# Optimization experiments

Measured on AMD Instinct MI355X. Metric: run time of the kernel, lower is better.

The kernel has to match this reference:

```python
import jax, jax.numpy as jnp
import numpy as np

N_FREQ = 256
N_CH = 256
VOCAB = 8192
B, T = 4, 2048


def gauss_proj(x, w, n_freq):
    # FFT over vocab dim, take first n_freq harmonics (skip DC), split real/imag
    X = jnp.fft.rfft(x, axis=-1)[..., 1:n_freq + 1]          # [B,T,n_freq] complex
    X_ri = jnp.concatenate([X.real, X.imag], axis=-1)         # [B,T,2*n_freq]
    return X_ri @ w.T                                         # [B,T,n_channels]


def gauss_synth(h, w, n_freq, V):
    Y_ri = h @ w                                              # [B,T,2*n_freq]
    Y = Y_ri[..., :n_freq] + 1j * Y_ri[..., n_freq:]          # [B,T,n_freq] complex
    full = jnp.zeros(h.shape[:-1] + (V // 2 + 1,), dtype=Y.dtype)
    full = full.at[..., 1:n_freq + 1].set(Y)                  # band-limited spectrum
    return jnp.fft.irfft(full, n=V, axis=-1)                  # [B,T,V]


def setup_inputs() -> dict:
    key = jax.random.key(0)
    ks = jax.random.split(key, 5)
    x = jax.random.normal(ks[0], (B, T, VOCAB), dtype=jnp.float32)
    q_w = jax.random.normal(ks[1], (N_CH, 2 * N_FREQ), dtype=jnp.float32) * 0.02
    k_w = jax.random.normal(ks[2], (N_CH, 2 * N_FREQ), dtype=jnp.float32) * 0.02
    v_w = jax.random.normal(ks[3], (N_CH, 2 * N_FREQ), dtype=jnp.float32) * 0.02
    o_w = jax.random.normal(ks[4], (N_CH, 2 * N_FREQ), dtype=jnp.float32) * 0.02
    decay_logit = jnp.float32(3.0)
    out_scale = jnp.float32(0.1)
    return {"x": x, "q_w": q_w, "k_w": k_w, "v_w": v_w, "o_w": o_w,
            "decay_logit": decay_logit, "out_scale": out_scale}


def reference(x, q_w, k_w, v_w, o_w, decay_logit, out_scale):
    q = gauss_proj(x, q_w, N_FREQ)                            # [B,T,C]
    k = gauss_proj(x, k_w, N_FREQ)
    v = gauss_proj(x, v_w, N_FREQ)
    scores = jnp.einsum('btc,bsc->bts', q, k)                 # [B,T,T]
    decay = jax.nn.sigmoid(decay_logit)
    t = x.shape[1]
    pos = jnp.arange(t)
    # faithful to torch: diff[t,s] = pos[s] - pos[t]
    diff = pos[None, :] - pos[:, None]
    weights = (decay ** jnp.clip(diff.astype(jnp.float32) - 1.0, 0.0)) * (diff > 0)
    scores = scores * weights[None, :, :]
    retrieved = jnp.einsum('bts,bsc->btc', scores, v)         # [B,T,C]
    return gauss_synth(retrieved, o_w, N_FREQ, VOCAB) * out_scale
```

## Files before the change

### kernel.cpp

```cpp
#include <hip/hip_runtime.h>
#include <hip/hip_bf16.h>
#include <cstdint>


typedef unsigned short u16;
typedef short short8 __attribute__((ext_vector_type(8)));
typedef float f32x4 __attribute__((ext_vector_type(4)));
typedef float f4 __attribute__((ext_vector_type(4)));

__device__ __forceinline__ u16 f2bf(float f) {
  union { float f; unsigned u; } v; v.f = f;
  unsigned u = v.u;
  u += 0x7fffu + ((u >> 16) & 1u);
  return (u16)(u >> 16);
}

__device__ __forceinline__ uint2 pack_bf4(f4 v) {
  union { u16 h[4]; uint2 q; } pk;
  pk.h[0] = f2bf(v[0]); pk.h[1] = f2bf(v[1]);
  pk.h[2] = f2bf(v[2]); pk.h[3] = f2bf(v[3]);
  return pk.q;
}

__device__ __forceinline__ void gload_lds16(const void* g, void* l) {
  __builtin_amdgcn_global_load_lds(
      (const __attribute__((address_space(1))) void*)g,
      (__attribute__((address_space(3))) void*)l, 16, 0, 0);
}

__global__ __launch_bounds__(256, 2)
void gemm_g1(const float* __restrict__ A, const u16* __restrict__ B,
             float* __restrict__ P)
{
  constexpr int NN = 512, KK = 8192, KC = 4096;
  constexpr int NT = KC / 32;

  __shared__ u16 As[2][128 * 32] __attribute__((aligned(16)));
  __shared__ u16 Bs[3][128 * 32] __attribute__((aligned(16)));

  const int tid  = threadIdx.x;
  const int wave = tid >> 6, lane = tid & 63;
  const int quad = lane >> 4, l15 = lane & 15;
  const int wm = wave >> 1, wn = wave & 1;

  const int lid = blockIdx.x;
  const int nat = (lid & 7) * 64 + (lid >> 3);
  const int y = nat >> 3, rem = nat & 7;
  const int x = rem & 3, z = rem >> 2;
  const int m0 = y * 128, n0 = x * 128, k00 = z * KC;

  const int loff0 = wave * 2048 + lane * 16;
  const int loff1 = loff0 + 1024;
  const int row0s = loff0 >> 6, kof0 = (loff0 & 63) >> 1;
  const int row1s = loff1 >> 6, kof1 = (loff1 & 63) >> 1;
  const u16* Bp0 = B + (size_t)(n0 + row0s) * KK + k00 + kof0;
  const u16* Bp1 = B + (size_t)(n0 + row1s) * KK + k00 + kof1;

  const int arow8 = tid >> 3;
  const int acol  = (tid & 7) * 4;
  const float* Ap = A + (size_t)(m0 + arow8) * KK + k00 + acol;

  f4 rv0[4], rv1[4];

#define ISSUE_A(RV, T)                                               \
  _Pragma("unroll")                                                  \
  for (int g = 0; g < 4; ++g)                                        \
    RV[g] = *(const f4*)(Ap + (size_t)g * 32 * KK + (size_t)(T) * 32);
#define ISSUE_B(T, SLOT)                                             \
  gload_lds16(Bp0 + (size_t)(T) * 32, (char*)Bs[SLOT] + loff0);      \
  gload_lds16(Bp1 + (size_t)(T) * 32, (char*)Bs[SLOT] + loff1);
#define CONVERT_A(RV, SLOT)                                          \
  _Pragma("unroll")                                                  \
  for (int g = 0; g < 4; ++g)                                        \
    *(uint2*)&As[SLOT][(g * 32 + arow8) * 32 + acol] = pack_bf4(RV[g]);
#define G1_COMPUTE(CUR, BSLOT)                                                   \
  {                                                                              \
    short8 a[4], b[4];                                                           \
    _Pragma("unroll")                                                            \
    for (int i = 0; i < 4; ++i)                                                  \
      a[i] = *(const short8*)&As[CUR][(wm * 64 + i * 16 + l15) * 32 + quad * 8]; \
    _Pragma("unroll")                                                            \
    for (int j = 0; j < 4; ++j)                                                  \
      b[j] = *(const short8*)&Bs[BSLOT][(wn * 64 + j * 16 + l15) * 32 + quad * 8]; \
    _Pragma("unroll")                                                            \
    for (int i = 0; i < 4; ++i)                                                  \
      _Pragma("unroll")                                                          \
      for (int j = 0; j < 4; ++j)                                                \
        acc[i][j] = __builtin_amdgcn_mfma_f32_16x16x32_bf16(a[i], b[j], acc[i][j], 0, 0, 0); \
  }
#define FENCE_BAR()                                                  \
  asm volatile("s_waitcnt vmcnt(6)" ::: "memory");                   \
  asm volatile("s_waitcnt lgkmcnt(0)" ::: "memory");                 \
  __builtin_amdgcn_s_barrier();                                      \
  asm volatile("" ::: "memory");

  ISSUE_A(rv0, 0);
  ISSUE_B(0, 0);
  ISSUE_A(rv1, 1);
  ISSUE_B(1, 1);
  CONVERT_A(rv0, 0);
  FENCE_BAR();

  f32x4 acc[4][4] = {};

#define BODY(T, RV_ISS, RV_CONV)                                     \
  {                                                                  \
    const int t2 = ((T) + 2 < NT) ? (T) + 2 : NT - 1;                \
    ISSUE_A(RV_ISS, t2);                                             \
    ISSUE_B(t2, ((T) + 2) % 3);                                      \
    G1_COMPUTE((T) & 1, (T) % 3);                                    \
    CONVERT_A(RV_CONV, ((T) + 1) & 1);                               \
    FENCE_BAR();                                                     \
  }

  for (int t = 0; t < NT; t += 2) {
    BODY(t, rv0, rv1);
    BODY(t + 1, rv1, rv0);
  }
#undef BODY
#undef FENCE_BAR
#undef G1_COMPUTE
#undef CONVERT_A
#undef ISSUE_B
#undef ISSUE_A

  float* Pz = P + (size_t)z * (8192L * 512);
  #pragma unroll
  for (int i = 0; i < 4; ++i) {
    #pragma unroll
    for (int j = 0; j < 4; ++j) {
      const int rb = m0 + wm * 64 + i * 16 + quad * 4;
      const int cc = n0 + wn * 64 + j * 16 + l15;
      #pragma unroll
      for (int r = 0; r < 4; ++r)
        Pz[(size_t)(rb + r) * NN + cc] = acc[i][j][r];
    }
  }
}

__global__ void reduce_cast(const float* __restrict__ P, u16* __restrict__ Xri) {
  const int i = blockIdx.x * 256 + threadIdx.x;
  const f4 a = ((const f4*)P)[i];
  const f4 b = ((const f4*)(P + 8192L * 512))[i];
  union { u16 h[4]; uint2 q; } pk;
  #pragma unroll
  for (int r = 0; r < 4; ++r) pk.h[r] = f2bf(a[r] + b[r]);
  ((uint2*)Xri)[i] = pk.q;
}

__global__ __launch_bounds__(256, 2)
void gemm_qkvw(const u16* __restrict__ Xri, const u16* __restrict__ Fm,
               const u16* __restrict__ qwb, const u16* __restrict__ kwb,
               const u16* __restrict__ vwb, const u16* __restrict__ owb,
               u16* __restrict__ Qb, u16* __restrict__ Kb,
               u16* __restrict__ Vt, u16* __restrict__ Wot)
{
  constexpr int N = 256, K = 512;
  __shared__ u16 As[128 * 32] __attribute__((aligned(16)));
  __shared__ u16 Bs[128 * 32] __attribute__((aligned(16)));

  const int tid  = threadIdx.x;
  const int wave = tid >> 6, lane = tid & 63;
  const int quad = lane >> 4, l15 = lane & 15;
  const int wm = wave >> 1, wn = wave & 1;
  const int m0 = blockIdx.y * 128, n0 = blockIdx.x * 128;
  const int z  = blockIdx.z;

  const u16* Ab = (z == 3) ? Fm : Xri;
  const u16* Bb = (z == 0) ? qwb : (z == 1) ? kwb : (z == 2) ? vwb : owb;
  const float alpha = (z == 3) ? (2.f / 8192.f) : 1.f;

  f32x4 acc[4][4] = {};

  const int loff0 = wave * 2048 + lane * 16;
  const int loff1 = loff0 + 1024;
  const int row0s = loff0 >> 6, kof0 = (loff0 & 63) >> 1;
  const int row1s = loff1 >> 6, kof1 = (loff1 & 63) >> 1;

  for (int k0 = 0; k0 < K; k0 += 32) {
    __syncthreads();
    gload_lds16(Ab + (size_t)(m0 + row0s) * K + k0 + kof0, (char*)As + loff0);
    gload_lds16(Ab + (size_t)(m0 + row1s) * K + k0 + kof1, (char*)As + loff1);
    gload_lds16(Bb + (size_t)(n0 + row0s) * K + k0 + kof0, (char*)Bs + loff0);
    gload_lds16(Bb + (size_t)(n0 + row1s) * K + k0 + kof1, (char*)Bs + loff1);
    __syncthreads();

    short8 a[4], b[4];
    #pragma unroll
    for (int i = 0; i < 4; ++i)
      a[i] = *(const short8*)&As[(wm * 64 + i * 16 + l15) * 32 + quad * 8];
    #pragma unroll
    for (int j = 0; j < 4; ++j)
      b[j] = *(const short8*)&Bs[(wn * 64 + j * 16 + l15) * 32 + quad * 8];
    #pragma unroll
    for (int i = 0; i < 4; ++i)
      #pragma unroll
      for (int j = 0; j < 4; ++j)
        acc[i][j] = __builtin_amdgcn_mfma_f32_16x16x32_bf16(a[i], b[j], acc[i][j], 0, 0, 0);
  }

  #pragma unroll
  for (int i = 0; i < 4; ++i) {
    #pragma unroll
    for (int j = 0; j < 4; ++j) {
      f32x4 v = acc[i][j];
      const int rb = m0 + wm * 64 + i * 16 + quad * 4;
      const int cc = n0 + wn * 64 + j * 16 + l15;
      if (z == 2) {
        const int bb = rb >> 11, ml = rb & 2047;
        union { u16 h[4]; uint2 q; } pk;
        #pragma unroll
        for (int r = 0; r < 4; ++r) pk.h[r] = f2bf(v[r]);
        *(uint2*)&Vt[((size_t)(bb << 8) + cc) * 2048 + ml] = pk.q;
      } else {
        u16* C = (z == 0) ? Qb : (z == 1) ? Kb : Wot;
        #pragma unroll
        for (int r = 0; r < 4; ++r)
          C[(size_t)(rb + r) * N + cc] = f2bf(v[r] * alpha);
      }
    }
  }
}

template<int EPI, bool AF32>
__global__ __launch_bounds__(256, 2)
void gemm_bt(const void* __restrict__ Av, const u16* __restrict__ B,
             void* __restrict__ Cv, int M, int N, int K,
             long sA, long sB, long sC,
             const float* __restrict__ scal, float alpha)
{
  __shared__ u16 As[128 * 32] __attribute__((aligned(16)));
  __shared__ u16 Bs[128 * 32] __attribute__((aligned(16)));

  const int tid  = threadIdx.x;
  const int wave = tid >> 6, lane = tid & 63;
  const int quad = lane >> 4, l15 = lane & 15;
  const int wm = wave >> 1, wn = wave & 1;
  const int m0 = blockIdx.y * 128, n0 = blockIdx.x * 128;
  const int z  = blockIdx.z;

  const u16*   Ab = (const u16*)Av + (size_t)z * sA;
  const float* Af = (const float*)Av + (size_t)z * sA;
  const u16*   Bb = B + (size_t)z * sB;

  f32x4 acc[4][4] = {};

  const int loff0 = wave * 2048 + lane * 16;
  const int loff1 = loff0 + 1024;
  const int row0s = loff0 >> 6, kof0 = (loff0 & 63) >> 1;
  const int row1s = loff1 >> 6, kof1 = (loff1 & 63) >> 1;

  for (int k0 = 0; k0 < K; k0 += 32) {
    __syncthreads();
    if (AF32) {
      const int row = tid >> 1, half = tid & 1;
      const float* ar = Af + (size_t)(m0 + row) * K + k0 + half * 16;
      f4 p0 = *(const f4*)(ar);
      f4 p1 = *(const f4*)(ar + 4);
      f4 p2 = *(const f4*)(ar + 8);
      f4 p3 = *(const f4*)(ar + 12);
      union { u16 h[16]; uint4 q[2]; } pk;
      #pragma unroll
      for (int e = 0; e < 4; ++e) {
        pk.h[e]      = f2bf(p0[e]);
        pk.h[4 + e]  = f2bf(p1[e]);
        pk.h[8 + e]  = f2bf(p2[e]);
        pk.h[12 + e] = f2bf(p3[e]);
      }
      uint4* dst = (uint4*)&As[row * 32 + half * 16];
      dst[0] = pk.q[0]; dst[1] = pk.q[1];
    } else {
      gload_lds16(Ab + (size_t)(m0 + row0s) * K + k0 + kof0, (char*)As + loff0);
      gload_lds16(Ab + (size_t)(m0 + row1s) * K + k0 + kof1, (char*)As + loff1);
    }
    gload_lds16(Bb + (size_t)(n0 + row0s) * K + k0 + kof0, (char*)Bs + loff0);
    gload_lds16(Bb + (size_t)(n0 + row1s) * K + k0 + kof1, (char*)Bs + loff1);
    __syncthreads();

    short8 a[4], b[4];
    #pragma unroll
    for (int i = 0; i < 4; ++i)
      a[i] = *(const short8*)&As[(wm * 64 + i * 16 + l15) * 32 + quad * 8];
    #pragma unroll
    for (int j = 0; j < 4; ++j)
      b[j] = *(const short8*)&Bs[(wn * 64 + j * 16 + l15) * 32 + quad * 8];
    #pragma unroll
    for (int i = 0; i < 4; ++i)
      #pragma unroll
      for (int j = 0; j < 4; ++j)
        acc[i][j] = __builtin_amdgcn_mfma_f32_16x16x32_bf16(a[i], b[j], acc[i][j], 0, 0, 0);
  }

  float dec_l2 = 0.f, oscale = 1.f;
  if (EPI == 3) {
    float logit = *scal;
    float dec = 1.f / (1.f + expf(-logit));
    dec_l2 = log2f(dec);
  }
  if (EPI == 4) oscale = *scal;

  #pragma unroll
  for (int i = 0; i < 4; ++i) {
    #pragma unroll
    for (int j = 0; j < 4; ++j) {
      f32x4 v = acc[i][j];
      const int rb = m0 + wm * 64 + i * 16 + quad * 4;
      const int cc = n0 + wn * 64 + j * 16 + l15;
      if (EPI == 0) {
        u16* C = (u16*)Cv + (size_t)z * sC;
        #pragma unroll
        for (int r = 0; r < 4; ++r)
          C[(size_t)(rb + r) * N + cc] = f2bf(v[r] * alpha);
      } else if (EPI == 2) {
        u16* C = (u16*)Cv;
        const int bb = rb >> 11, ml = rb & 2047;
        union { u16 h[4]; uint2 q; } pk;
        #pragma unroll
        for (int r = 0; r < 4; ++r) pk.h[r] = f2bf(v[r]);
        *(uint2*)&C[((size_t)(bb << 8) + cc) * 2048 + ml] = pk.q;
      } else if (EPI == 3) {
        u16* C = (u16*)Cv + (size_t)z * sC;
        #pragma unroll
        for (int r = 0; r < 4; ++r) {
          const int d = cc - (rb + r);
          float w = (d > 0) ? exp2f(dec_l2 * (float)(d - 1)) : 0.f;
          C[(size_t)(rb + r) * N + cc] = f2bf(v[r] * w);
        }
      } else if (EPI == 4) {
        float* C = (float*)Cv;
        #pragma unroll
        for (int r = 0; r < 4; ++r)
          C[(size_t)(rb + r) * N + cc] = v[r] * oscale;
      }
    }
  }
}

__global__ void genF_row(u16* Fm) {
  int idx = blockIdx.x * 256 + threadIdx.x;
  int n = idx >> 9, j = idx & 511;
  int k = (j & 255) + 1;
  int ph = (n * k) & 8191;
  float ang = (float)ph * 7.66990393942820795e-4f;
  float s, c; sincosf(ang, &s, &c);
  Fm[idx] = f2bf(j < 256 ? c : -s);
}
__global__ void genF_col(u16* Ft) {
  int idx = blockIdx.x * 256 + threadIdx.x;
  int j = idx >> 13, n = idx & 8191;
  int k = (j & 255) + 1;
  int ph = (n * k) & 8191;
  float ang = (float)ph * 7.66990393942820795e-4f;
  float s, c; sincosf(ang, &s, &c);
  Ft[idx] = f2bf(j < 256 ? c : -s);
}

__global__ void cast_w4(const float* a, const float* b, const float* c, const float* d,
                        u16* oa, u16* ob, u16* oc, u16* od) {
  int i = blockIdx.x * 256 + threadIdx.x;
  oa[i] = f2bf(a[i]); ob[i] = f2bf(b[i]); oc[i] = f2bf(c[i]); od[i] = f2bf(d[i]);
}

extern "C" void kernel_launch(void* const* d_in, const int* in_sizes, int n_in,
                              void* d_out, int out_size, void* d_ws, size_t ws_size,
                              hipStream_t stream)
{
  const float* x  = (const float*)d_in[0];
  const float* qw = (const float*)d_in[1];
  const float* kw = (const float*)d_in[2];
  const float* vw = (const float*)d_in[3];
  const float* ow = (const float*)d_in[4];
  const float* dl = (const float*)d_in[5];
  const float* os = (const float*)d_in[6];
  float* out = (float*)d_out;

  char* W = (char*)d_ws;
  const size_t MB = 1024 * 1024;
  u16* Fm  = (u16*)(W);
  u16* Ft  = (u16*)(W + 8 * MB);
  u16* Xri = (u16*)(W + 16 * MB);
  u16* Qb  = (u16*)(W + 24 * MB);
  u16* Kb  = (u16*)(W + 28 * MB);
  u16* Vt  = (u16*)(W + 32 * MB);
  u16* Wot = (u16*)(W + 36 * MB);
  u16* S   = (u16*)(W + 40 * MB);
  float* P = (float*)(W + 40 * MB);
  u16* R   = (u16*)(W + 72 * MB);
  u16* qwb = (u16*)(W + 76 * MB);
  u16* kwb = qwb + 131072;
  u16* vwb = kwb + 131072;
  u16* owb = vwb + 131072;

  genF_row<<<8192 * 512 / 256, 256, 0, stream>>>(Fm);
  genF_col<<<8192 * 512 / 256, 256, 0, stream>>>(Ft);
  cast_w4<<<131072 / 256, 256, 0, stream>>>(qw, kw, vw, ow, qwb, kwb, vwb, owb);

  gemm_g1<<<512, 256, 0, stream>>>(x, Ft, P);
  reduce_cast<<<4096, 256, 0, stream>>>(P, Xri);

  gemm_qkvw<<<dim3(2, 64, 4), 256, 0, stream>>>(Xri, Fm, qwb, kwb, vwb, owb,
                                                Qb, Kb, Vt, Wot);

  gemm_bt<3, false><<<dim3(16, 16, 4), 256, 0, stream>>>(Qb, Kb, S, 2048, 2048, 256,
                                                         2048L * 256, 2048L * 256, 2048L * 2048, dl, 1.f);
  gemm_bt<0, false><<<dim3(2, 16, 4), 256, 0, stream>>>(S, Vt, R, 2048, 256, 2048,
                                                        2048L * 2048, 256L * 2048, 2048L * 256, nullptr, 1.f);
  gemm_bt<4, false><<<dim3(64, 64, 1), 256, 0, stream>>>(R, Wot, out, 8192, 8192, 256, 0, 0, 0, os, 1.f);
}
```

Baseline: 680.5 us.

## Skip zero triangle in score and retrieval GEMMs; deepen K tile in spectral GEMM

The QK^T score GEMM now skips output tiles below the diagonal, since the causal decay mask makes them zero. The S·V GEMM is replaced by a split-K kernel that starts each row block's K loop at the diagonal, writes fp32 partials and reduces them with a generalized reduce_cast. Separately, the rfft-projection GEMM moves to a 64-wide K tile with XOR-swizzled LDS layout and double buffering of B, reorganizing its load/compute schedule. The changes cut wasted MFMA work and loop overhead, but add an extra reduction pass and reuse the Fm/Ft workspace for partials.

```diff
diff --git a/kernel.cpp b/kernel.cpp
--- a/kernel.cpp
+++ b/kernel.cpp
@@ -33,15 +33,16 @@
              float* __restrict__ P)
 {
   constexpr int NN = 512, KK = 8192, KC = 4096;
-  constexpr int NT = KC / 32;
-
-  __shared__ u16 As[2][128 * 32] __attribute__((aligned(16)));
-  __shared__ u16 Bs[3][128 * 32] __attribute__((aligned(16)));
+  constexpr int NT = KC / 64;
+
+  __shared__ u16 As[2][128 * 64] __attribute__((aligned(16)));
+  __shared__ u16 Bs[2][128 * 64] __attribute__((aligned(16)));
 
   const int tid  = threadIdx.x;
   const int wave = tid >> 6, lane = tid & 63;
   const int quad = lane >> 4, l15 = lane & 15;
   const int wm = wave >> 1, wn = wave & 1;
+  const int swz8 = (l15 & 7) << 3;
 
   const int lid = blockIdx.x;
   const int nat = (lid & 7) * 64 + (lid >> 3);
@@ -49,55 +50,61 @@
   const int x = rem & 3, z = rem >> 2;
   const int m0 = y * 128, n0 = x * 128, k00 = z * KC;
 
-  const int loff0 = wave * 2048 + lane * 16;
-  const int loff1 = loff0 + 1024;
-  const int row0s = loff0 >> 6, kof0 = (loff0 & 63) >> 1;
-  const int row1s = loff1 >> 6, kof1 = (loff1 & 63) >> 1;
-  const u16* Bp0 = B + (size_t)(n0 + row0s) * KK + k00 + kof0;
-  const u16* Bp1 = B + (size_t)(n0 + row1s) * KK + k00 + kof1;
-
-  const int arow8 = tid >> 3;
-  const int acol  = (tid & 7) * 4;
-  const float* Ap = A + (size_t)(m0 + arow8) * KK + k00 + acol;
-
-  f4 rv0[4], rv1[4];
+  const int brow = tid >> 3;
+  const int bswz = ((tid & 7) * 8) ^ (((tid >> 3) & 7) << 3);
+  const u16* Bp = B + (size_t)(n0 + brow) * KK + k00 + bswz;
+  const int bloff = tid * 16;
+
+  const int arow16 = tid >> 4;
+  const int acolf  = (tid & 15) * 4;
+  const float* Ap = A + (size_t)(m0 + arow16) * KK + k00 + acolf;
+  const int awz = ((tid & 15) * 4) ^ (((tid >> 4) & 7) << 3);
+
+  f4 rv0[8], rv1[8];
 
 #define ISSUE_A(RV, T)                                               \
   _Pragma("unroll")                                                  \
-  for (int g = 0; g < 4; ++g)                                        \
-    RV[g] = *(const f4*)(Ap + (size_t)g * 32 * KK + (size_t)(T) * 32);
+  for (int g = 0; g < 8; ++g)                                        \
+    RV[g] = *(const f4*)(Ap + (size_t)g * 16 * KK + (size_t)(T) * 64);
 #define ISSUE_B(T, SLOT)                                             \
-  gload_lds16(Bp0 + (size_t)(T) * 32, (char*)Bs[SLOT] + loff0);      \
-  gload_lds16(Bp1 + (size_t)(T) * 32, (char*)Bs[SLOT] + loff1);
+  _Pragma("unroll")                                                  \
+  for (int h = 0; h < 4; ++h)                                        \
+    gload_lds16(Bp + (size_t)h * 32 * KK + (size_t)(T) * 64,         \
+                (char*)Bs[SLOT] + h * 4096 + bloff);
 #define CONVERT_A(RV, SLOT)                                          \
   _Pragma("unroll")                                                  \
-  for (int g = 0; g < 4; ++g)                                        \
-    *(uint2*)&As[SLOT][(g * 32 + arow8) * 32 + acol] = pack_bf4(RV[g]);
-#define G1_COMPUTE(CUR, BSLOT)                                                   \
-  {                                                                              \
+  for (int g = 0; g < 8; ++g)                                        \
+    *(uint2*)&As[SLOT][(g * 16 + arow16) * 64 + awz] = pack_bf4(RV[g]);
+#define G1_COMPUTE(CUR)                                                          \
+  _Pragma("unroll")                                                              \
+  for (int ks = 0; ks < 2; ++ks) {                                               \
     short8 a[4], b[4];                                                           \
     _Pragma("unroll")                                                            \
     for (int i = 0; i < 4; ++i)                                                  \
-      a[i] = *(const short8*)&As[CUR][(wm * 64 + i * 16 + l15) * 32 + quad * 8]; \
+      a[i] = *(const short8*)&As[CUR][(wm * 64 + i * 16 + l15) * 64 +            \
+                                      ((ks * 32 + quad * 8) ^ swz8)];            \
     _Pragma("unroll")                                                            \
     for (int j = 0; j < 4; ++j)                                                  \
-      b[j] = *(const short8*)&Bs[BSLOT][(wn * 64 + j * 16 + l15) * 32 + quad * 8]; \
+      b[j] = *(const short8*)&Bs[CUR][(wn * 64 + j * 16 + l15) * 64 +            \
+                                      ((ks * 32 + quad * 8) ^ swz8)];            \
     _Pragma("unroll")                                                            \
     for (int i = 0; i < 4; ++i)                                                  \
       _Pragma("unroll")                                                          \
       for (int j = 0; j < 4; ++j)                                                \
         acc[i][j] = __builtin_amdgcn_mfma_f32_16x16x32_bf16(a[i], b[j], acc[i][j], 0, 0, 0); \
   }
+#define SB() __builtin_amdgcn_sched_barrier(0)
 #define FENCE_BAR()                                                  \
-  asm volatile("s_waitcnt vmcnt(6)" ::: "memory");                   \
+  asm volatile("s_waitcnt vmcnt(8)" ::: "memory");                   \
   asm volatile("s_waitcnt lgkmcnt(0)" ::: "memory");                 \
   __builtin_amdgcn_s_barrier();                                      \
   asm volatile("" ::: "memory");
 
   ISSUE_A(rv0, 0);
   ISSUE_B(0, 0);
+  SB();
   ISSUE_A(rv1, 1);
-  ISSUE_B(1, 1);
+  SB();
   CONVERT_A(rv0, 0);
   FENCE_BAR();
 
@@ -106,9 +113,11 @@
 #define BODY(T, RV_ISS, RV_CONV)                                     \
   {                                                                  \
     const int t2 = ((T) + 2 < NT) ? (T) + 2 : NT - 1;                \
+    ISSUE_B((T) + 1 < NT ? (T) + 1 : NT - 1, ((T) + 1) & 1);         \
+    SB();                                                            \
     ISSUE_A(RV_ISS, t2);                                             \
-    ISSUE_B(t2, ((T) + 2) % 3);                                      \
-    G1_COMPUTE((T) & 1, (T) % 3);                                    \
+    SB();                                                            \
+    G1_COMPUTE((T) & 1);                                             \
     CONVERT_A(RV_CONV, ((T) + 1) & 1);                               \
     FENCE_BAR();                                                     \
   }
@@ -119,6 +128,7 @@
   }
 #undef BODY
 #undef FENCE_BAR
+#undef SB
 #undef G1_COMPUTE
 #undef CONVERT_A
 #undef ISSUE_B
@@ -138,14 +148,15 @@
   }
 }
 
-__global__ void reduce_cast(const float* __restrict__ P, u16* __restrict__ Xri) {
+__global__ void reduce_cast(const float* __restrict__ P, u16* __restrict__ O,
+                            int half_f4) {
   const int i = blockIdx.x * 256 + threadIdx.x;
   const f4 a = ((const f4*)P)[i];
-  const f4 b = ((const f4*)(P + 8192L * 512))[i];
+  const f4 b = ((const f4*)P)[i + half_f4];
   union { u16 h[4]; uint2 q; } pk;
   #pragma unroll
   for (int r = 0; r < 4; ++r) pk.h[r] = f2bf(a[r] + b[r]);
-  ((uint2*)Xri)[i] = pk.q;
+  ((uint2*)O)[i] = pk.q;
 }
 
 __global__ __launch_bounds__(256, 2)
@@ -222,13 +233,80 @@
   }
 }
 
-template<int EPI, bool AF32>
+__global__ __launch_bounds__(256, 2)
+void gemm_g5(const u16* __restrict__ S, const u16* __restrict__ Vt,
+             float* __restrict__ P5)
+{
+  constexpr int N = 256, K = 2048;
+  __shared__ u16 As[128 * 32] __attribute__((aligned(16)));
+  __shared__ u16 Bs[128 * 32] __attribute__((aligned(16)));
+
+  const int tid  = threadIdx.x;
+  const int wave = tid >> 6, lane = tid & 63;
+  const int quad = lane >> 4, l15 = lane & 15;
+  const int wm = wave >> 1, wn = wave & 1;
+  const int m0 = blockIdx.y * 128, n0 = blockIdx.x * 128;
+  const int batch = blockIdx.z & 3, half = blockIdx.z >> 2;
+
+  const u16* Ab = S  + (size_t)batch * 2048 * 2048;
+  const u16* Bb = Vt + (size_t)batch * 256 * 2048;
+
+  int kbeg = half * 1024;
+  if (m0 > kbeg) kbeg = m0;
+  const int kend = half * 1024 + 1024;
+
+  f32x4 acc[4][4] = {};
+
+  const int loff0 = wave * 2048 + lane * 16;
+  const int loff1 = loff0 + 1024;
+  const int row0s = loff0 >> 6, kof0 = (loff0 & 63) >> 1;
+  const int row1s = loff1 >> 6, kof1 = (loff1 & 63) >> 1;
+
+  for (int k0 = kbeg; k0 < kend; k0 += 32) {
+    __syncthreads();
+    gload_lds16(Ab + (size_t)(m0 + row0s) * K + k0 + kof0, (char*)As + loff0);
+    gload_lds16(Ab + (size_t)(m0 + row1s) * K + k0 + kof1, (char*)As + loff1);
+    gload_lds16(Bb + (size_t)(n0 + row0s) * K + k0 + kof0, (char*)Bs + loff0);
+    gload_lds16(Bb + (size_t)(n0 + row1s) * K + k0 + kof1, (char*)Bs + loff1);
+    __syncthreads();
+
+    short8 a[4], b[4];
+    #pragma unroll
+    for (int i = 0; i < 4; ++i)
+      a[i] = *(const short8*)&As[(wm * 64 + i * 16 + l15) * 32 + quad * 8];
+    #pragma unroll
+    for (int j = 0; j < 4; ++j)
+      b[j] = *(const short8*)&Bs[(wn * 64 + j * 16 + l15) * 32 + quad * 8];
+    #pragma unroll
+    for (int i = 0; i < 4; ++i)
+      #pragma unroll
+      for (int j = 0; j < 4; ++j)
+        acc[i][j] = __builtin_amdgcn_mfma_f32_16x16x32_bf16(a[i], b[j], acc[i][j], 0, 0, 0);
+  }
+
+  float* Pz = P5 + (size_t)half * (8192L * 256) + (size_t)batch * 2048 * 256;
+  #pragma unroll
+  for (int i = 0; i < 4; ++i) {
+    #pragma unroll
+    for (int j = 0; j < 4; ++j) {
+      const int rb = m0 + wm * 64 + i * 16 + quad * 4;
+      const int cc = n0 + wn * 64 + j * 16 + l15;
+      #pragma unroll
+      for (int r = 0; r < 4; ++r)
+        Pz[(size_t)(rb + r) * N + cc] = acc[i][j][r];
+    }
+  }
+}
+
+template<int EPI, bool AF32, bool TRI>
 __global__ __launch_bounds__(256, 2)
 void gemm_bt(const void* __restrict__ Av, const u16* __restrict__ B,
              void* __restrict__ Cv, int M, int N, int K,
              long sA, long sB, long sC,
              const float* __restrict__ scal, float alpha)
 {
+  if (TRI && blockIdx.x < blockIdx.y) return;
+
   __shared__ u16 As[128 * 32] __attribute__((aligned(16)));
   __shared__ u16 Bs[128 * 32] __attribute__((aligned(16)));
 
@@ -311,13 +389,6 @@
         #pragma unroll
         for (int r = 0; r < 4; ++r)
           C[(size_t)(rb + r) * N + cc] = f2bf(v[r] * alpha);
-      } else if (EPI == 2) {
-        u16* C = (u16*)Cv;
-        const int bb = rb >> 11, ml = rb & 2047;
-        union { u16 h[4]; uint2 q; } pk;
-        #pragma unroll
-        for (int r = 0; r < 4; ++r) pk.h[r] = f2bf(v[r]);
-        *(uint2*)&C[((size_t)(bb << 8) + cc) * 2048 + ml] = pk.q;
       } else if (EPI == 3) {
         u16* C = (u16*)Cv + (size_t)z * sC;
         #pragma unroll
@@ -385,6 +456,7 @@
   u16* Wot = (u16*)(W + 36 * MB);
   u16* S   = (u16*)(W + 40 * MB);
   float* P = (float*)(W + 40 * MB);
+  float* P5 = (float*)(W);
   u16* R   = (u16*)(W + 72 * MB);
   u16* qwb = (u16*)(W + 76 * MB);
   u16* kwb = qwb + 131072;
@@ -396,14 +468,15 @@
   cast_w4<<<131072 / 256, 256, 0, stream>>>(qw, kw, vw, ow, qwb, kwb, vwb, owb);
 
   gemm_g1<<<512, 256, 0, stream>>>(x, Ft, P);
-  reduce_cast<<<4096, 256, 0, stream>>>(P, Xri);
+  reduce_cast<<<4096, 256, 0, stream>>>(P, Xri, 8192 * 512 / 4);
 
   gemm_qkvw<<<dim3(2, 64, 4), 256, 0, stream>>>(Xri, Fm, qwb, kwb, vwb, owb,
                                                 Qb, Kb, Vt, Wot);
 
-  gemm_bt<3, false><<<dim3(16, 16, 4), 256, 0, stream>>>(Qb, Kb, S, 2048, 2048, 256,
-                                                         2048L * 256, 2048L * 256, 2048L * 2048, dl, 1.f);
-  gemm_bt<0, false><<<dim3(2, 16, 4), 256, 0, stream>>>(S, Vt, R, 2048, 256, 2048,
-                                                        2048L * 2048, 256L * 2048, 2048L * 256, nullptr, 1.f);
-  gemm_bt<4, false><<<dim3(64, 64, 1), 256, 0, stream>>>(R, Wot, out, 8192, 8192, 256, 0, 0, 0, os, 1.f);
-}
+  gemm_bt<3, false, true><<<dim3(16, 16, 4), 256, 0, stream>>>(Qb, Kb, S, 2048, 2048, 256,
+                                                               2048L * 256, 2048L * 256, 2048L * 2048, dl, 1.f);
+  gemm_g5<<<dim3(2, 16, 8), 256, 0, stream>>>(S, Vt, P5);
+  reduce_cast<<<2048, 256, 0, stream>>>(P5, R, 8192 * 256 / 4);
+
+  gemm_bt<4, false, false><<<dim3(64, 64, 1), 256, 0, stream>>>(R, Wot, out, 8192, 8192, 256, 0, 0, 0, os, 1.f);
+}
```

After: 624.5 us. 8.2% less time.
